# Kernel tuning notes

Hardware: AMD Instinct MI355X
Metric: run time of the kernel (lower is better)

## Reference

```python
import jax, jax.numpy as jnp
import numpy as np

D_IN, D_K, D_V = 1024, 1024, 1024
B, S = 4, 2048

def setup_inputs() -> dict:
    key = jax.random.key(0)
    ks = jax.random.split(key, 7)
    s = 1.0 / np.sqrt(D_IN)
    return {
        "x": jax.random.normal(ks[0], (B, S, D_IN), dtype=jnp.float32),
        "Wq": jax.random.uniform(ks[1], (D_IN, D_K), jnp.float32, -s, s),
        "bq": jax.random.uniform(ks[2], (D_K,), jnp.float32, -s, s),
        "Wk": jax.random.uniform(ks[3], (D_IN, D_K), jnp.float32, -s, s),
        "bk": jax.random.uniform(ks[4], (D_K,), jnp.float32, -s, s),
        "Wv": jax.random.uniform(ks[5], (D_IN, D_V), jnp.float32, -s, s),
        "bv": jax.random.uniform(ks[6], (D_V,), jnp.float32, -s, s),
    }

def reference(x, Wq, bq, Wk, bk, Wv, bv):
    # QKV projections: [B,S,d_in] @ [d_in,d] + b
    Q = x @ Wq + bq  # [B,S,d_k]
    K = x @ Wk + bk  # [B,S,d_k]
    V = x @ Wv + bv  # [B,S,d_v]
    # Non-standard recipe: softmax over UNSCALED scores, then divide output by sqrt(d_k)
    scores = jnp.einsum('bqd,bkd->bqk', Q, K)  # [B,S,S]
    attn = jax.nn.softmax(scores, axis=2)
    out = jnp.einsum('bqk,bkv->bqv', attn, V) / jnp.sqrt(jnp.asarray(K.shape[2], dtype=x.dtype))
    return out
```

## Files before the change

### kernel.cpp

```cpp
#include <hip/hip_runtime.h>
#include <stdint.h>

typedef unsigned short u16;
typedef _Float16 f16;
typedef _Float16 f16x8 __attribute__((ext_vector_type(8)));
typedef float f32x4 __attribute__((ext_vector_type(4)));

#define DIN 1024
#define SEQ 2048
#define NB 4
#define MB (1u << 20)


__device__ __forceinline__ void gload_lds16(const void* g, void* l) {
    __builtin_amdgcn_global_load_lds(
        (__attribute__((address_space(1))) void*)(uintptr_t)g,
        (__attribute__((address_space(3))) void*)l,
        16, 0, 0);
}


__device__ __forceinline__ void gemm_tile(
    const char* __restrict__ A, const char* __restrict__ B,
    int lda, int ldb, int ksteps, char* smem, f32x4 acc[4][4])
{
    const int lane = threadIdx.x & 63;
    const int wave = threadIdx.x >> 6;

    #pragma unroll
    for (int m = 0; m < 4; ++m)
        #pragma unroll
        for (int n = 0; n < 4; ++n)
            acc[m][n] = (f32x4){0.f, 0.f, 0.f, 0.f};

    const char* ga[4];
    const char* gb[4];
    int ldsoff[4];
    #pragma unroll
    for (int i = 0; i < 4; ++i) {
        int La = (wave * 4 + i) * 1024 + lane * 16;
        int r  = La >> 7;
        int cb = La & 127;
        int sc = cb ^ ((r & 7) << 4);
        ga[i] = A + (size_t)r * (size_t)(lda * 2) + sc;
        gb[i] = B + (size_t)r * (size_t)(ldb * 2) + sc;
        ldsoff[i] = (wave * 4 + i) * 1024;
    }

    const int wr = (wave >> 1) * 64;
    const int wc = (wave & 1) * 64;

    for (int ks = 0; ks < ksteps; ++ks) {
        #pragma unroll
        for (int i = 0; i < 4; ++i) {
            gload_lds16(ga[i], smem + ldsoff[i]);
            gload_lds16(gb[i], smem + 16384 + ldsoff[i]);
            ga[i] += 128;
            gb[i] += 128;
        }
        __syncthreads();

        #pragma unroll
        for (int kk = 0; kk < 2; ++kk) {
            const int kb = kk * 64 + ((lane >> 4) << 4);
            f16x8 af[4], bfv[4];
            #pragma unroll
            for (int m = 0; m < 4; ++m) {
                int r = wr + m * 16 + (lane & 15);
                af[m] = *(const f16x8*)(smem + r * 128 + (kb ^ ((r & 7) << 4)));
            }
            #pragma unroll
            for (int n = 0; n < 4; ++n) {
                int r = wc + n * 16 + (lane & 15);
                bfv[n] = *(const f16x8*)(smem + 16384 + r * 128 + (kb ^ ((r & 7) << 4)));
            }
            #pragma unroll
            for (int m = 0; m < 4; ++m)
                #pragma unroll
                for (int n = 0; n < 4; ++n)
                    acc[m][n] = __builtin_amdgcn_mfma_f32_16x16x32_f16(
                        af[m], bfv[n], acc[m][n], 0, 0, 0);
        }
        __syncthreads();
    }
}


__global__ void k_convx(const float* __restrict__ x, f16* __restrict__ xh, int n8) {
    int idx = blockIdx.x * blockDim.x + threadIdx.x;
    int stride = gridDim.x * blockDim.x;
    for (; idx < n8; idx += stride) {
        f32x4 a = ((const f32x4*)x)[(size_t)idx * 2];
        f32x4 b = ((const f32x4*)x)[(size_t)idx * 2 + 1];
        f16x8 o;
        o[0] = (f16)a[0]; o[1] = (f16)a[1]; o[2] = (f16)a[2]; o[3] = (f16)a[3];
        o[4] = (f16)b[0]; o[5] = (f16)b[1]; o[6] = (f16)b[2]; o[7] = (f16)b[3];
        ((f16x8*)xh)[idx] = o;
    }
}

__global__ void k_wt(const float* __restrict__ Wq, const float* __restrict__ Wk,
                     const float* __restrict__ Wv, f16* __restrict__ Wt) {
    __shared__ float tile[32][33];
    const int mtx = blockIdx.z;
    const float* W = (mtx == 0) ? Wq : (mtx == 1 ? Wk : Wv);
    const int n0 = blockIdx.x * 32, k0 = blockIdx.y * 32;
    const int c = threadIdx.x & 31, r0 = threadIdx.x >> 5;
    #pragma unroll
    for (int rr = r0; rr < 32; rr += 8)
        tile[rr][c] = W[(size_t)(k0 + rr) * DIN + n0 + c];
    __syncthreads();
    f16* o = Wt + (size_t)mtx * DIN * DIN;
    #pragma unroll
    for (int rr = r0; rr < 32; rr += 8)
        o[(size_t)(n0 + rr) * DIN + k0 + c] = (f16)tile[c][rr];
}

__global__ __launch_bounds__(256) void k_gemm_qkv(
    const f16* __restrict__ xh, const f16* __restrict__ wt,
    const float* __restrict__ bq, const float* __restrict__ bk,
    const float* __restrict__ bv,
    f16* __restrict__ Q, f16* __restrict__ K, f16* __restrict__ V)
{
    __shared__ __align__(16) char smem[32768];
    f32x4 acc[4][4];
    const int blkN = blockIdx.x;
    const int blkM = blockIdx.y;
    gemm_tile((const char*)(xh + (size_t)blkM * 128 * DIN),
              (const char*)(wt + (size_t)blkN * 128 * DIN),
              DIN, DIN, DIN / 64, smem, acc);

    const int lane = threadIdx.x & 63;
    const int wave = threadIdx.x >> 6;
    const int row0 = blkM * 128 + (wave >> 1) * 64;
    const int col0 = blkN * 128 + (wave & 1) * 64;
    #pragma unroll
    for (int n = 0; n < 4; ++n) {
        int col = col0 + n * 16 + (lane & 15);
        int nb = col >> 10, nc = col & 1023;
        const float* bsrc = (nb == 0) ? bq : (nb == 1 ? bk : bv);
        float bias = bsrc[nc];
        f16* dst = (nb == 0) ? Q : (nb == 1 ? K : V);
        #pragma unroll
        for (int m = 0; m < 4; ++m) {
            #pragma unroll
            for (int j = 0; j < 4; ++j) {
                int row = row0 + m * 16 + (lane >> 4) * 4 + j;
                dst[(size_t)row * 1024 + nc] = (f16)(acc[m][n][j] + bias);
            }
        }
    }
}

__global__ void k_transpose_v(const u16* __restrict__ V, u16* __restrict__ Vt) {
    __shared__ u16 tile[32][33];
    const int b = blockIdx.z;
    const int s0 = blockIdx.x * 32, d0 = blockIdx.y * 32;
    const int c = threadIdx.x & 31, r0 = threadIdx.x >> 5;
    const u16* Vb = V + (size_t)b * SEQ * 1024;
    u16* Vtb = Vt + (size_t)b * 1024 * SEQ;
    #pragma unroll
    for (int rr = r0; rr < 32; rr += 8)
        tile[rr][c] = Vb[(size_t)(s0 + rr) * 1024 + d0 + c];
    __syncthreads();
    #pragma unroll
    for (int rr = r0; rr < 32; rr += 8)
        Vtb[(size_t)(d0 + rr) * SEQ + s0 + c] = tile[c][rr];
}

__global__ __launch_bounds__(256) void k_gemm_scores(
    const f16* __restrict__ Q, const f16* __restrict__ K, float* __restrict__ S)
{
    __shared__ __align__(16) char smem[32768];
    f32x4 acc[4][4];
    const int b = blockIdx.z;
    const f16* Qb = Q + (size_t)b * SEQ * 1024;
    const f16* Kb = K + (size_t)b * SEQ * 1024;
    gemm_tile((const char*)(Qb + (size_t)blockIdx.y * 128 * 1024),
              (const char*)(Kb + (size_t)blockIdx.x * 128 * 1024),
              1024, 1024, 1024 / 64, smem, acc);

    float* Sb = S + (size_t)b * SEQ * SEQ;
    const int lane = threadIdx.x & 63;
    const int wave = threadIdx.x >> 6;
    const int row0 = blockIdx.y * 128 + (wave >> 1) * 64;
    const int col0 = blockIdx.x * 128 + (wave & 1) * 64;
    #pragma unroll
    for (int m = 0; m < 4; ++m)
        #pragma unroll
        for (int n = 0; n < 4; ++n) {
            int col = col0 + n * 16 + (lane & 15);
            #pragma unroll
            for (int j = 0; j < 4; ++j) {
                int row = row0 + m * 16 + (lane >> 4) * 4 + j;
                Sb[(size_t)row * SEQ + col] = acc[m][n][j];
            }
        }
}

__global__ __launch_bounds__(256) void k_softmax(
    const float* __restrict__ S, f16* __restrict__ P)
{
    const size_t row = blockIdx.x;
    const float* s = S + row * SEQ;
    f16* p = P + row * SEQ;
    const int t = threadIdx.x;

    f32x4 x0 = ((const f32x4*)s)[t * 2];
    f32x4 x1 = ((const f32x4*)s)[t * 2 + 1];
    float v[8] = {x0[0], x0[1], x0[2], x0[3], x1[0], x1[1], x1[2], x1[3]};

    float mx = v[0];
    #pragma unroll
    for (int j = 1; j < 8; ++j) mx = fmaxf(mx, v[j]);
    #pragma unroll
    for (int o = 32; o; o >>= 1) mx = fmaxf(mx, __shfl_xor(mx, o, 64));
    __shared__ float red[8];
    if ((t & 63) == 0) red[t >> 6] = mx;
    __syncthreads();
    mx = fmaxf(fmaxf(red[0], red[1]), fmaxf(red[2], red[3]));

    float sum = 0.f;
    #pragma unroll
    for (int j = 0; j < 8; ++j) { v[j] = __expf(v[j] - mx); sum += v[j]; }
    #pragma unroll
    for (int o = 32; o; o >>= 1) sum += __shfl_xor(sum, o, 64);
    if ((t & 63) == 0) red[4 + (t >> 6)] = sum;
    __syncthreads();
    sum = (red[4] + red[5]) + (red[6] + red[7]);
    float inv = 1.0f / sum;

    f16x8 o8;
    #pragma unroll
    for (int j = 0; j < 8; ++j) o8[j] = (f16)(v[j] * inv);
    ((f16x8*)p)[t] = o8;
}

__global__ __launch_bounds__(256) void k_gemm_pv(
    const f16* __restrict__ P, const f16* __restrict__ Vt, float* __restrict__ out)
{
    __shared__ __align__(16) char smem[32768];
    f32x4 acc[4][4];
    const int b = blockIdx.z;
    const f16* Pb  = P  + (size_t)b * SEQ * SEQ;
    const f16* Vtb = Vt + (size_t)b * 1024 * SEQ;
    gemm_tile((const char*)(Pb  + (size_t)blockIdx.y * 128 * SEQ),
              (const char*)(Vtb + (size_t)blockIdx.x * 128 * SEQ),
              SEQ, SEQ, SEQ / 64, smem, acc);

    float* ob = out + (size_t)b * SEQ * 1024;
    const int lane = threadIdx.x & 63;
    const int wave = threadIdx.x >> 6;
    const int row0 = blockIdx.y * 128 + (wave >> 1) * 64;
    const int col0 = blockIdx.x * 128 + (wave & 1) * 64;
    #pragma unroll
    for (int m = 0; m < 4; ++m)
        #pragma unroll
        for (int n = 0; n < 4; ++n) {
            int col = col0 + n * 16 + (lane & 15);
            #pragma unroll
            for (int j = 0; j < 4; ++j) {
                int row = row0 + m * 16 + (lane >> 4) * 4 + j;
                ob[(size_t)row * 1024 + col] = acc[m][n][j] * 0.03125f;
            }
        }
}


extern "C" void kernel_launch(void* const* d_in, const int* in_sizes, int n_in,
                              void* d_out, int out_size, void* d_ws, size_t ws_size,
                              hipStream_t stream) {
    const float* x  = (const float*)d_in[0];
    const float* Wq = (const float*)d_in[1];
    const float* bq = (const float*)d_in[2];
    const float* Wk = (const float*)d_in[3];
    const float* bk = (const float*)d_in[4];
    const float* Wv = (const float*)d_in[5];
    const float* bv = (const float*)d_in[6];
    float* out = (float*)d_out;
    char* ws = (char*)d_ws;

    f16*  Q  = (f16*)(ws);
    f16*  K  = (f16*)(ws + (size_t)16 * MB);
    f16*  V  = (f16*)(ws + (size_t)32 * MB);
    f16*  Vt = (f16*)(ws + (size_t)48 * MB);
    f16*  xh = (f16*)(ws + (size_t)64 * MB);
    f16*  wt = (f16*)(ws + (size_t)80 * MB);
    float* S = (float*)(ws + (size_t)64 * MB);
    f16*  P  = Q;

    const size_t needed = (size_t)128 * MB;
    if (ws_size < needed) return;

    k_convx<<<2048, 256, 0, stream>>>(x, xh, (NB * SEQ * DIN) / 8);
    k_wt<<<dim3(32, 32, 3), 256, 0, stream>>>(Wq, Wk, Wv, wt);
    k_gemm_qkv<<<dim3(24, 64), 256, 0, stream>>>(xh, wt, bq, bk, bv, Q, K, V);
    k_transpose_v<<<dim3(SEQ / 32, 1024 / 32, NB), 256, 0, stream>>>((const u16*)V, (u16*)Vt);
    k_gemm_scores<<<dim3(SEQ / 128, SEQ / 128, NB), 256, 0, stream>>>(Q, K, S);
    k_softmax<<<NB * SEQ, 256, 0, stream>>>(S, P);
    k_gemm_pv<<<dim3(1024 / 128, SEQ / 128, NB), 256, 0, stream>>>(P, Vt, out);
}
```

Before: 191.8 us.

## Fuse prep kernels, write V transposed from QKV GEMM, add XCD swizzle

Merges the x conversion and weight transpose into one launch, and drops the separate V-transpose kernel by having the QKV GEMM epilogue write V directly in transposed layout. It also remaps 1D block indices with an XCD-aware swizzle in all three GEMMs so neighbouring tiles land on the same XCD and share L2. This removes two launches and one full read/write pass over V. The transposed V store is strided along the sequence dimension, which may coalesce poorly.

```diff
diff --git a/kernel.cpp b/kernel.cpp
--- a/kernel.cpp
+++ b/kernel.cpp
@@ -17,6 +17,10 @@
         (__attribute__((address_space(1))) void*)(uintptr_t)g,
         (__attribute__((address_space(3))) void*)l,
         16, 0, 0);
+}
+
+__device__ __forceinline__ int xcd_swz(int h, int cpx) {
+    return (h & 7) * cpx + (h >> 3);
 }
 
 
@@ -86,46 +90,52 @@
 }
 
 
-__global__ void k_convx(const float* __restrict__ x, f16* __restrict__ xh, int n8) {
-    int idx = blockIdx.x * blockDim.x + threadIdx.x;
-    int stride = gridDim.x * blockDim.x;
-    for (; idx < n8; idx += stride) {
-        f32x4 a = ((const f32x4*)x)[(size_t)idx * 2];
-        f32x4 b = ((const f32x4*)x)[(size_t)idx * 2 + 1];
-        f16x8 o;
-        o[0] = (f16)a[0]; o[1] = (f16)a[1]; o[2] = (f16)a[2]; o[3] = (f16)a[3];
-        o[4] = (f16)b[0]; o[5] = (f16)b[1]; o[6] = (f16)b[2]; o[7] = (f16)b[3];
-        ((f16x8*)xh)[idx] = o;
+__global__ __launch_bounds__(256) void k_prep(
+    const float* __restrict__ x, f16* __restrict__ xh,
+    const float* __restrict__ Wq, const float* __restrict__ Wk,
+    const float* __restrict__ Wv, f16* __restrict__ wt)
+{
+    __shared__ float tile[32][33];
+    const int bid = blockIdx.x;
+    if (bid < 2048) {
+        const int n8 = (NB * SEQ * DIN) / 8;
+        for (int idx = bid * 256 + threadIdx.x; idx < n8; idx += 2048 * 256) {
+            f32x4 a = ((const f32x4*)x)[(size_t)idx * 2];
+            f32x4 b = ((const f32x4*)x)[(size_t)idx * 2 + 1];
+            f16x8 o;
+            o[0] = (f16)a[0]; o[1] = (f16)a[1]; o[2] = (f16)a[2]; o[3] = (f16)a[3];
+            o[4] = (f16)b[0]; o[5] = (f16)b[1]; o[6] = (f16)b[2]; o[7] = (f16)b[3];
+            ((f16x8*)xh)[idx] = o;
+        }
+    } else {
+        const int wb = bid - 2048;
+        const int mtx = wb >> 10;
+        const int rem = wb & 1023;
+        const int n0 = (rem & 31) * 32, k0 = (rem >> 5) * 32;
+        const float* W = (mtx == 0) ? Wq : (mtx == 1 ? Wk : Wv);
+        const int c = threadIdx.x & 31, r0 = threadIdx.x >> 5;
+        #pragma unroll
+        for (int rr = r0; rr < 32; rr += 8)
+            tile[rr][c] = W[(size_t)(k0 + rr) * DIN + n0 + c];
+        __syncthreads();
+        f16* o = wt + (size_t)mtx * DIN * DIN;
+        #pragma unroll
+        for (int rr = r0; rr < 32; rr += 8)
+            o[(size_t)(n0 + rr) * DIN + k0 + c] = (f16)tile[c][rr];
     }
-}
-
-__global__ void k_wt(const float* __restrict__ Wq, const float* __restrict__ Wk,
-                     const float* __restrict__ Wv, f16* __restrict__ Wt) {
-    __shared__ float tile[32][33];
-    const int mtx = blockIdx.z;
-    const float* W = (mtx == 0) ? Wq : (mtx == 1 ? Wk : Wv);
-    const int n0 = blockIdx.x * 32, k0 = blockIdx.y * 32;
-    const int c = threadIdx.x & 31, r0 = threadIdx.x >> 5;
-    #pragma unroll
-    for (int rr = r0; rr < 32; rr += 8)
-        tile[rr][c] = W[(size_t)(k0 + rr) * DIN + n0 + c];
-    __syncthreads();
-    f16* o = Wt + (size_t)mtx * DIN * DIN;
-    #pragma unroll
-    for (int rr = r0; rr < 32; rr += 8)
-        o[(size_t)(n0 + rr) * DIN + k0 + c] = (f16)tile[c][rr];
 }
 
 __global__ __launch_bounds__(256) void k_gemm_qkv(
     const f16* __restrict__ xh, const f16* __restrict__ wt,
     const float* __restrict__ bq, const float* __restrict__ bk,
     const float* __restrict__ bv,
-    f16* __restrict__ Q, f16* __restrict__ K, f16* __restrict__ V)
+    f16* __restrict__ Q, f16* __restrict__ K, f16* __restrict__ Vt)
 {
     __shared__ __align__(16) char smem[32768];
     f32x4 acc[4][4];
-    const int blkN = blockIdx.x;
-    const int blkM = blockIdx.y;
+    const int sid = xcd_swz(blockIdx.x, 192);
+    const int blkN = sid % 24;
+    const int blkM = sid / 24;
     gemm_tile((const char*)(xh + (size_t)blkM * 128 * DIN),
               (const char*)(wt + (size_t)blkN * 128 * DIN),
               DIN, DIN, DIN / 64, smem, acc);
@@ -134,38 +144,42 @@
     const int wave = threadIdx.x >> 6;
     const int row0 = blkM * 128 + (wave >> 1) * 64;
     const int col0 = blkN * 128 + (wave & 1) * 64;
-    #pragma unroll
-    for (int n = 0; n < 4; ++n) {
-        int col = col0 + n * 16 + (lane & 15);
-        int nb = col >> 10, nc = col & 1023;
-        const float* bsrc = (nb == 0) ? bq : (nb == 1 ? bk : bv);
-        float bias = bsrc[nc];
-        f16* dst = (nb == 0) ? Q : (nb == 1 ? K : V);
-        #pragma unroll
-        for (int m = 0; m < 4; ++m) {
-            #pragma unroll
-            for (int j = 0; j < 4; ++j) {
-                int row = row0 + m * 16 + (lane >> 4) * 4 + j;
-                dst[(size_t)row * 1024 + nc] = (f16)(acc[m][n][j] + bias);
+
+    if (col0 >= 2048) {
+        const int bb = row0 >> 11;
+        const int sb = row0 & (SEQ - 1);
+        f16* Vtb = Vt + (size_t)bb * DIN * SEQ;
+        #pragma unroll
+        for (int n = 0; n < 4; ++n) {
+            int d = (col0 - 2048) + n * 16 + (lane & 15);
+            float bias = bv[d];
+            #pragma unroll
+            for (int m = 0; m < 4; ++m) {
+                #pragma unroll
+                for (int j = 0; j < 4; ++j) {
+                    int s = sb + m * 16 + (lane >> 4) * 4 + j;
+                    Vtb[(size_t)d * SEQ + s] = (f16)(acc[m][n][j] + bias);
+                }
+            }
+        }
+    } else {
+        f16* dst = (col0 < 1024) ? Q : K;
+        const float* bsrc = (col0 < 1024) ? bq : bk;
+        const int ncb = col0 & 1023;
+        #pragma unroll
+        for (int n = 0; n < 4; ++n) {
+            int nc = ncb + n * 16 + (lane & 15);
+            float bias = bsrc[nc];
+            #pragma unroll
+            for (int m = 0; m < 4; ++m) {
+                #pragma unroll
+                for (int j = 0; j < 4; ++j) {
+                    int row = row0 + m * 16 + (lane >> 4) * 4 + j;
+                    dst[(size_t)row * 1024 + nc] = (f16)(acc[m][n][j] + bias);
+                }
             }
         }
     }
-}
-
-__global__ void k_transpose_v(const u16* __restrict__ V, u16* __restrict__ Vt) {
-    __shared__ u16 tile[32][33];
-    const int b = blockIdx.z;
-    const int s0 = blockIdx.x * 32, d0 = blockIdx.y * 32;
-    const int c = threadIdx.x & 31, r0 = threadIdx.x >> 5;
-    const u16* Vb = V + (size_t)b * SEQ * 1024;
-    u16* Vtb = Vt + (size_t)b * 1024 * SEQ;
-    #pragma unroll
-    for (int rr = r0; rr < 32; rr += 8)
-        tile[rr][c] = Vb[(size_t)(s0 + rr) * 1024 + d0 + c];
-    __syncthreads();
-    #pragma unroll
-    for (int rr = r0; rr < 32; rr += 8)
-        Vtb[(size_t)(d0 + rr) * SEQ + s0 + c] = tile[c][rr];
 }
 
 __global__ __launch_bounds__(256) void k_gemm_scores(
@@ -173,18 +187,21 @@
 {
     __shared__ __align__(16) char smem[32768];
     f32x4 acc[4][4];
-    const int b = blockIdx.z;
+    const int sid = xcd_swz(blockIdx.x, 128);
+    const int bx = sid & 15;
+    const int by = (sid >> 4) & 15;
+    const int b  = sid >> 8;
     const f16* Qb = Q + (size_t)b * SEQ * 1024;
     const f16* Kb = K + (size_t)b * SEQ * 1024;
-    gemm_tile((const char*)(Qb + (size_t)blockIdx.y * 128 * 1024),
-              (const char*)(Kb + (size_t)blockIdx.x * 128 * 1024),
+    gemm_tile((const char*)(Qb + (size_t)by * 128 * 1024),
+              (const char*)(Kb + (size_t)bx * 128 * 1024),
               1024, 1024, 1024 / 64, smem, acc);
 
     float* Sb = S + (size_t)b * SEQ * SEQ;
     const int lane = threadIdx.x & 63;
     const int wave = threadIdx.x >> 6;
-    const int row0 = blockIdx.y * 128 + (wave >> 1) * 64;
-    const int col0 = blockIdx.x * 128 + (wave & 1) * 64;
+    const int row0 = by * 128 + (wave >> 1) * 64;
+    const int col0 = bx * 128 + (wave & 1) * 64;
     #pragma unroll
     for (int m = 0; m < 4; ++m)
         #pragma unroll
@@ -241,18 +258,21 @@
 {
     __shared__ __align__(16) char smem[32768];
     f32x4 acc[4][4];
-    const int b = blockIdx.z;
+    const int sid = xcd_swz(blockIdx.x, 64);
+    const int bx = sid & 7;
+    const int by = (sid >> 3) & 15;
+    const int b  = sid >> 7;
     const f16* Pb  = P  + (size_t)b * SEQ * SEQ;
     const f16* Vtb = Vt + (size_t)b * 1024 * SEQ;
-    gemm_tile((const char*)(Pb  + (size_t)blockIdx.y * 128 * SEQ),
-              (const char*)(Vtb + (size_t)blockIdx.x * 128 * SEQ),
+    gemm_tile((const char*)(Pb  + (size_t)by * 128 * SEQ),
+              (const char*)(Vtb + (size_t)bx * 128 * SEQ),
               SEQ, SEQ, SEQ / 64, smem, acc);
 
     float* ob = out + (size_t)b * SEQ * 1024;
     const int lane = threadIdx.x & 63;
     const int wave = threadIdx.x >> 6;
-    const int row0 = blockIdx.y * 128 + (wave >> 1) * 64;
-    const int col0 = blockIdx.x * 128 + (wave & 1) * 64;
+    const int row0 = by * 128 + (wave >> 1) * 64;
+    const int col0 = bx * 128 + (wave & 1) * 64;
     #pragma unroll
     for (int m = 0; m < 4; ++m)
         #pragma unroll
@@ -282,21 +302,18 @@
 
     f16*  Q  = (f16*)(ws);
     f16*  K  = (f16*)(ws + (size_t)16 * MB);
-    f16*  V  = (f16*)(ws + (size_t)32 * MB);
-    f16*  Vt = (f16*)(ws + (size_t)48 * MB);
-    f16*  xh = (f16*)(ws + (size_t)64 * MB);
-    f16*  wt = (f16*)(ws + (size_t)80 * MB);
-    float* S = (float*)(ws + (size_t)64 * MB);
+    f16*  Vt = (f16*)(ws + (size_t)32 * MB);
+    f16*  xh = (f16*)(ws + (size_t)48 * MB);
+    f16*  wt = (f16*)(ws + (size_t)64 * MB);
+    float* S = (float*)(ws + (size_t)48 * MB);
     f16*  P  = Q;
 
-    const size_t needed = (size_t)128 * MB;
+    const size_t needed = (size_t)112 * MB;
     if (ws_size < needed) return;
 
-    k_convx<<<2048, 256, 0, stream>>>(x, xh, (NB * SEQ * DIN) / 8);
-    k_wt<<<dim3(32, 32, 3), 256, 0, stream>>>(Wq, Wk, Wv, wt);
-    k_gemm_qkv<<<dim3(24, 64), 256, 0, stream>>>(xh, wt, bq, bk, bv, Q, K, V);
-    k_transpose_v<<<dim3(SEQ / 32, 1024 / 32, NB), 256, 0, stream>>>((const u16*)V, (u16*)Vt);
-    k_gemm_scores<<<dim3(SEQ / 128, SEQ / 128, NB), 256, 0, stream>>>(Q, K, S);
+    k_prep<<<5120, 256, 0, stream>>>(x, xh, Wq, Wk, Wv, wt);
+    k_gemm_qkv<<<1536, 256, 0, stream>>>(xh, wt, bq, bk, bv, Q, K, Vt);
+    k_gemm_scores<<<1024, 256, 0, stream>>>(Q, K, S);
     k_softmax<<<NB * SEQ, 256, 0, stream>>>(S, P);
-    k_gemm_pv<<<dim3(1024 / 128, SEQ / 128, NB), 256, 0, stream>>>(P, Vt, out);
-}
+    k_gemm_pv<<<512, 256, 0, stream>>>(P, Vt, out);
+}
```

Result: faster. 173.5 us (-9.5%).
